# Performance work log

Hardware: AMD Instinct MI355X
Metric: run time of the kernel (lower is better)

## Reference

```python
import jax, jax.numpy as jnp
import numpy as np

EPS = 1e-5
ALPHA = 1.0

def _conv1x1(x, w, b):
    # x: [N,C,T,V], w: [O,C], b: [O] -> [N,O,T,V]
    return jnp.einsum('nctv,oc->notv', x, w) + b[None, :, None, None]

def _groupnorm1(x, gamma, beta):
    # GroupNorm(1, C): normalize over (C,T,V) per sample
    mu = jnp.mean(x, axis=(1, 2, 3), keepdims=True)
    var = jnp.var(x, axis=(1, 2, 3), keepdims=True)
    xn = (x - mu) * jax.lax.rsqrt(var + EPS)
    return xn * gamma[None, :, None, None] + beta[None, :, None, None]

def setup_inputs() -> dict:
    key = jax.random.key(0)
    ks = jax.random.split(key, 12)
    N, Cin, T, V, O, R = 128, 64, 128, 25, 64, 8
    s_in = 1.0 / np.sqrt(Cin)
    s_r = 1.0 / np.sqrt(R)
    return {
        'x':  jax.random.normal(ks[0], (N, Cin, T, V), jnp.float32),
        'A':  jax.random.normal(ks[1], (V, V), jnp.float32) * 0.1,
        'w1': jax.random.normal(ks[2], (R, Cin), jnp.float32) * s_in,
        'b1': jnp.zeros((R,), jnp.float32),
        'g1': jnp.ones((R,), jnp.float32),
        'be1': jnp.zeros((R,), jnp.float32),
        'w2': jax.random.normal(ks[3], (R, Cin), jnp.float32) * s_in,
        'b2': jnp.zeros((R,), jnp.float32),
        'g2': jnp.ones((R,), jnp.float32),
        'be2': jnp.zeros((R,), jnp.float32),
        'w3': jax.random.normal(ks[4], (O, Cin), jnp.float32) * s_in,
        'b3': jnp.zeros((O,), jnp.float32),
        'w4': jax.random.normal(ks[5], (O, R), jnp.float32) * s_r,
        'b4': jnp.zeros((O,), jnp.float32),
    }

def reference(x, A, w1, b1, g1, be1, w2, b2, g2, be2, w3, b3, w4, b4):
    # branch 1: conv1 -> GroupNorm -> temporal mean -> pairwise diff -> tanh
    x1 = _groupnorm1(_conv1x1(x, w1, b1), g1, be1).mean(axis=2)      # [N,R,V]
    y1 = jnp.tanh(x1[..., :, None] - x1[..., None, :])               # [N,R,V,V]
    # branch 2: conv2 -> GroupNorm -> temporal mean -> outer product -> tanh
    x2 = _groupnorm1(_conv1x1(x, w2, b2), g2, be2).mean(axis=2)      # [N,R,V]
    y2 = jnp.tanh(x2[..., :, None] * x2[..., None, :])               # [N,R,V,V]
    # value branch
    x3 = _conv1x1(x, w3, b3)                                          # [N,O,T,V]
    # dynamic adjacency: conv4 over rel channels
    ys = y1 + ALPHA * y2 + A[None, None]                              # [N,R,V,V]
    y_sum = jnp.einsum('nruv,or->nouv', ys, w4) + b4[None, :, None, None]
    # aggregation over vertices
    y = jnp.einsum('ncuv,nctv->nctu', y_sum, x3)                      # [N,O,T,V]
    return y
```

## Files before the change

### kernel.cpp

```cpp
#include <hip/hip_runtime.h>

#define EPSV 1e-5f
constexpr int NN = 128, CIN = 64, TT = 128, VV = 25, OO = 64, RR = 8;
constexpr int TVQ   = TT * VV;
constexpr int XSAMP = CIN * TVQ;
constexpr int YSAMP = OO * TT * VV;
constexpr int RTV   = RR * TT * VV;
constexpr int S12N  = 2 * RR * VV;
constexpr int YST_SAMP = VV * VV * OO;
constexpr int X3_SAMP  = TVQ * OO;

__global__ __launch_bounds__(256) void kZero(float* __restrict__ p, int n)
{
    int i = blockIdx.x * 256 + threadIdx.x;
    if (i < n) p[i] = 0.f;
}

__global__ __launch_bounds__(256) void kA(const float* __restrict__ x,
    const float* __restrict__ w1, const float* __restrict__ b1,
    const float* __restrict__ w2, const float* __restrict__ b2,
    float* __restrict__ s12g, float* __restrict__ ssqg)
{
    __shared__ float wt1[CIN * RR], wt2[CIN * RR];
    __shared__ float s1l[RR * VV], s2l[RR * VV];
    __shared__ float redA[4], redB[4];
    const int tid = threadIdx.x;
    const int tc  = blockIdx.x;
    const int n   = blockIdx.y;

    for (int e = tid; e < CIN * RR; e += 256) {
        int r = e >> 6, c = e & 63;
        wt1[c * RR + r] = w1[e];
        wt2[c * RR + r] = w2[e];
    }
    for (int e = tid; e < 2 * RR * VV; e += 256) {
        if (e < RR * VV) s1l[e] = 0.f; else s2l[e - RR * VV] = 0.f;
    }
    __syncthreads();

    float acc1[4][RR], acc2[4][RR];
    #pragma unroll
    for (int j = 0; j < 4; ++j)
        #pragma unroll
        for (int r = 0; r < RR; ++r) { acc1[j][r] = 0.f; acc2[j][r] = 0.f; }

    const bool active = (tid < 200);
    const int p0 = tid * 4;
    const float* xb = x + (size_t)n * XSAMP + tc * 800 + p0;
    if (active) {
        #pragma unroll 4
        for (int c = 0; c < CIN; ++c) {
            float4 xv  = *(const float4*)(xb + c * TVQ);
            float4 wa1 = *(const float4*)(&wt1[c * RR]);
            float4 wb1 = *(const float4*)(&wt1[c * RR + 4]);
            float4 wa2 = *(const float4*)(&wt2[c * RR]);
            float4 wb2 = *(const float4*)(&wt2[c * RR + 4]);
            float xj[4]  = {xv.x, xv.y, xv.z, xv.w};
            float w1v[8] = {wa1.x, wa1.y, wa1.z, wa1.w, wb1.x, wb1.y, wb1.z, wb1.w};
            float w2v[8] = {wa2.x, wa2.y, wa2.z, wa2.w, wb2.x, wb2.y, wb2.z, wb2.w};
            #pragma unroll
            for (int j = 0; j < 4; ++j)
                #pragma unroll
                for (int r = 0; r < RR; ++r) {
                    acc1[j][r] += w1v[r] * xj[j];
                    acc2[j][r] += w2v[r] * xj[j];
                }
        }
    }

    float b1r[RR], b2r[RR];
    #pragma unroll
    for (int r = 0; r < RR; ++r) { b1r[r] = b1[r]; b2r[r] = b2[r]; }

    float ssq1 = 0.f, ssq2 = 0.f;
    if (active) {
        #pragma unroll
        for (int j = 0; j < 4; ++j) {
            int v = (p0 + j) % VV;
            #pragma unroll
            for (int r = 0; r < RR; ++r) {
                float c1 = acc1[j][r] + b1r[r]; ssq1 += c1 * c1;
                float c2 = acc2[j][r] + b2r[r]; ssq2 += c2 * c2;
                atomicAdd(&s1l[r * VV + v], acc1[j][r]);
                atomicAdd(&s2l[r * VV + v], acc2[j][r]);
            }
        }
    }
    #pragma unroll
    for (int off = 32; off > 0; off >>= 1) {
        ssq1 += __shfl_down(ssq1, off);
        ssq2 += __shfl_down(ssq2, off);
    }
    if ((tid & 63) == 0) { redA[tid >> 6] = ssq1; redB[tid >> 6] = ssq2; }
    __syncthreads();
    for (int e = tid; e < S12N; e += 256) {
        float pv = (e < RR * VV) ? s1l[e] : s2l[e - RR * VV];
        atomicAdd(&s12g[n * S12N + e], pv);
    }
    if (tid == 0) {
        atomicAdd(&ssqg[n * 2 + 0], redA[0] + redA[1] + redA[2] + redA[3]);
        atomicAdd(&ssqg[n * 2 + 1], redB[0] + redB[1] + redB[2] + redB[3]);
    }
}

__device__ __forceinline__ float tanh_fast(float v)
{
    float e = __expf(2.f * v);
    return 1.f - 2.f / (e + 1.f);
}

__global__ __launch_bounds__(512) void kB(
    const float* __restrict__ s12g, const float* __restrict__ ssqg,
    const float* __restrict__ b1, const float* __restrict__ g1, const float* __restrict__ be1,
    const float* __restrict__ b2, const float* __restrict__ g2, const float* __restrict__ be2,
    const float* __restrict__ Amat, const float* __restrict__ w4, const float* __restrict__ b4,
    float* __restrict__ ysumT)
{
    __shared__ float x1g[RR * VV], x2g[RR * VV];
    __shared__ float w4l[OO * RR];
    __shared__ float b4l[OO];
    __shared__ float stats[2];
    __shared__ float mss[4];
    const int tid = threadIdx.x;
    const int bx  = blockIdx.x;
    const int n   = blockIdx.y;

    if (tid < 2) stats[tid] = 0.f;
    if (tid < OO * RR) w4l[tid] = w4[tid];
    if (tid < OO) b4l[tid] = b4[tid];
    __syncthreads();

    float sv = 0.f;
    if (tid < S12N) {
        sv = s12g[n * S12N + tid];
        atomicAdd(&stats[tid / (RR * VV)], sv);
    }
    __syncthreads();
    if (tid == 0) {
        float sb1 = 0.f, sb2 = 0.f;
        for (int r = 0; r < RR; ++r) { sb1 += b1[r]; sb2 += b2[r]; }
        float mu1 = (stats[0] + (float)(TT * VV) * sb1) / (float)RTV;
        float mu2 = (stats[1] + (float)(TT * VV) * sb2) / (float)RTV;
        float var1 = ssqg[n * 2 + 0] / (float)RTV - mu1 * mu1;
        float var2 = ssqg[n * 2 + 1] / (float)RTV - mu2 * mu2;
        mss[0] = mu1; mss[1] = rsqrtf(var1 + EPSV);
        mss[2] = mu2; mss[3] = rsqrtf(var2 + EPSV);
    }
    __syncthreads();
    if (tid < S12N) {
        int br = tid / (RR * VV);
        int i  = tid % (RR * VV);
        int r  = i / VV;
        float mu = mss[br * 2], rs = mss[br * 2 + 1];
        float mean_t = sv / (float)TT + (br ? b2[r] : b1[r]);
        float g  = br ? g2[r]  : g1[r];
        float be = br ? be2[r] : be1[r];
        float val = g * (mean_t - mu) * rs + be;
        if (br == 0) x1g[i] = val; else x2g[i] = val;
    }
    __syncthreads();

    float* yn = ysumT + (size_t)n * YST_SAMP;
    const int pend = (bx + 1) * 125;
    for (int p = bx * 125 + tid; p < pend; p += 512) {
        int u = p / VV, v = p % VV;
        float Av = Amat[p];
        float ys[RR];
        #pragma unroll
        for (int r = 0; r < RR; ++r) {
            float d = x1g[r * VV + u] - x1g[r * VV + v];
            float m = x2g[r * VV + u] * x2g[r * VV + v];
            ys[r] = tanh_fast(d) + tanh_fast(m) + Av;
        }
        float* dst = yn + (size_t)p * OO;
        for (int o = 0; o < OO; ++o) {
            float a = b4l[o];
            #pragma unroll
            for (int r = 0; r < RR; ++r) a += w4l[o * RR + r] * ys[r];
            dst[o] = a;
        }
    }
}

__global__ __launch_bounds__(256) void kC1(const float* __restrict__ x,
    const float* __restrict__ w3, const float* __restrict__ b3,
    float* __restrict__ x3T)
{
    __shared__ float wt[CIN * 68];
    const int tid = threadIdx.x;
    const int n   = blockIdx.y;
    const int oq  = tid & 7;
    const int pg  = tid >> 3;
    const int p0  = blockIdx.x * 256 + pg * 8;

    for (int e = tid; e < CIN * OO; e += 256) {
        int o = e >> 6, c = e & 63;
        wt[c * 68 + o] = w3[e];
    }
    __syncthreads();

    float acc[8][8];
    #pragma unroll
    for (int i = 0; i < 8; ++i)
        #pragma unroll
        for (int j = 0; j < 8; ++j) acc[i][j] = 0.f;

    const bool act = (p0 < TVQ);
    const float* xp = x + (size_t)n * XSAMP + p0;
    if (act) {
        #pragma unroll 4
        for (int c = 0; c < CIN; ++c) {
            const float* xc = xp + c * TVQ;
            float4 xa = *(const float4*)(xc);
            float4 xb = *(const float4*)(xc + 4);
            const float* wr = &wt[c * 68 + oq * 8];
            float4 wa = *(const float4*)(wr);
            float4 wb = *(const float4*)(wr + 4);
            float xv[8] = {xa.x, xa.y, xa.z, xa.w, xb.x, xb.y, xb.z, xb.w};
            float wv[8] = {wa.x, wa.y, wa.z, wa.w, wb.x, wb.y, wb.z, wb.w};
            #pragma unroll
            for (int i = 0; i < 8; ++i)
                #pragma unroll
                for (int j = 0; j < 8; ++j)
                    acc[i][j] += wv[i] * xv[j];
        }
    }

    float bo[8];
    #pragma unroll
    for (int i = 0; i < 8; ++i) bo[i] = b3[oq * 8 + i];
    if (act) {
        float* dst = x3T + (size_t)n * X3_SAMP + (size_t)p0 * OO + oq * 8;
        #pragma unroll
        for (int j = 0; j < 8; ++j) {
            float4 s0, s1;
            s0.x = acc[0][j] + bo[0]; s0.y = acc[1][j] + bo[1];
            s0.z = acc[2][j] + bo[2]; s0.w = acc[3][j] + bo[3];
            s1.x = acc[4][j] + bo[4]; s1.y = acc[5][j] + bo[5];
            s1.z = acc[6][j] + bo[6]; s1.w = acc[7][j] + bo[7];
            *(float4*)(dst + j * OO)     = s0;
            *(float4*)(dst + j * OO + 4) = s1;
        }
    }
}

__global__ __launch_bounds__(256) void kC2(const float* __restrict__ x3T,
    const float* __restrict__ ysumT, float* __restrict__ y)
{
    __shared__ float lds[OO * 101];
    const int tid = threadIdx.x;
    const int tc  = blockIdx.x;
    const int n   = blockIdx.y;
    const int t0  = tc * 8;
    const int o2  = tid & 63;
    const int th2 = tid >> 6;

    const float* xb = x3T + (size_t)n * X3_SAMP;
    float acc2[2][VV];
    #pragma unroll
    for (int row = 0; row < 2; ++row) {
        const int t = t0 + 2 * th2 + row;
        #pragma unroll
        for (int v = 0; v < VV; ++v)
            acc2[row][v] = xb[(size_t)(t * VV + v) * OO + o2];
    }

    const float* yT = ysumT + (size_t)n * YST_SAMP + o2;
    float res[2][VV];
    #pragma unroll
    for (int u = 0; u < VV; ++u) {
        float r0 = 0.f, r1 = 0.f;
        #pragma unroll
        for (int v = 0; v < VV; ++v) {
            float yv = yT[(u * VV + v) * OO];
            r0 += yv * acc2[0][v];
            r1 += yv * acc2[1][v];
        }
        res[0][u] = r0;
        res[1][u] = r1;
    }

    float* yb = y + (size_t)n * YSAMP + t0 * VV;
    #pragma unroll 1
    for (int half = 0; half < 2; ++half) {
        __syncthreads();
        if ((th2 >> 1) == half) {
            #pragma unroll
            for (int row = 0; row < 2; ++row) {
                const int tl = (2 * th2 + row) & 3;
                #pragma unroll
                for (int u = 0; u < VV; ++u)
                    lds[o2 * 101 + tl * VV + u] = res[row][u];
            }
        }
        __syncthreads();
        for (int e = tid; e < 6400; e += 256) {
            int o = e / 100, m = e % 100;
            yb[o * TVQ + half * 100 + m] = lds[o * 101 + m];
        }
    }
}

__global__ __launch_bounds__(256) void kC(
    const float* __restrict__ x, const float* __restrict__ w3,
    const float* __restrict__ b3, const float* __restrict__ ysumT,
    float* __restrict__ y)
{
    __shared__ float lds[7168];
    const int tid = threadIdx.x;
    const int tc  = blockIdx.x;
    const int n   = blockIdx.y;
    const int t0  = tc * 8;

    const int og = tid >> 3;
    const int th = tid & 7;
    const int o0 = og * 2;

    float acc[2][VV];
    #pragma unroll
    for (int j = 0; j < 2; ++j)
        #pragma unroll
        for (int v = 0; v < VV; ++v) acc[j][v] = 0.f;

    const float* xn = x + (size_t)n * XSAMP + t0 * VV;
    #pragma unroll 1
    for (int cpass = 0; cpass < 2; ++cpass) {
        __syncthreads();
        for (int e4 = tid; e4 < 32 * 50; e4 += 256) {
            int cl = e4 / 50, r4 = (e4 % 50) * 4;
            float4 tv = *(const float4*)(xn + (cpass * 32 + cl) * TVQ + r4);
            float a[4] = {tv.x, tv.y, tv.z, tv.w};
            #pragma unroll
            for (int j = 0; j < 4; ++j) {
                int rem = r4 + j;
                lds[cl * 224 + (rem / VV) * 28 + (rem % VV)] = a[j];
            }
        }
        __syncthreads();
        #pragma unroll 1
        for (int q = 0; q < 2; ++q) {
            float w3q[2][16];
            #pragma unroll
            for (int j = 0; j < 2; ++j)
                #pragma unroll
                for (int k4 = 0; k4 < 4; ++k4) {
                    float4 wv = *(const float4*)(w3 + (o0 + j) * CIN
                                                 + cpass * 32 + q * 16 + k4 * 4);
                    w3q[j][k4*4+0] = wv.x; w3q[j][k4*4+1] = wv.y;
                    w3q[j][k4*4+2] = wv.z; w3q[j][k4*4+3] = wv.w;
                }
            #pragma unroll
            for (int ci = 0; ci < 16; ++ci) {
                const float* p = &lds[(q * 16 + ci) * 224 + th * 28];
                float4 a0 = *(const float4*)(p + 0);
                float4 a1 = *(const float4*)(p + 4);
                float4 a2 = *(const float4*)(p + 8);
                float4 a3 = *(const float4*)(p + 12);
                float4 a4 = *(const float4*)(p + 16);
                float4 a5 = *(const float4*)(p + 20);
                float  a6 = p[24];
                #pragma unroll
                for (int j = 0; j < 2; ++j) {
                    const float w = w3q[j][ci];
                    float* a = acc[j];
                    a[0]  += w*a0.x; a[1]  += w*a0.y; a[2]  += w*a0.z; a[3]  += w*a0.w;
                    a[4]  += w*a1.x; a[5]  += w*a1.y; a[6]  += w*a1.z; a[7]  += w*a1.w;
                    a[8]  += w*a2.x; a[9]  += w*a2.y; a[10] += w*a2.z; a[11] += w*a2.w;
                    a[12] += w*a3.x; a[13] += w*a3.y; a[14] += w*a3.z; a[15] += w*a3.w;
                    a[16] += w*a4.x; a[17] += w*a4.y; a[18] += w*a4.z; a[19] += w*a4.w;
                    a[20] += w*a5.x; a[21] += w*a5.y; a[22] += w*a5.z; a[23] += w*a5.w;
                    a[24] += w*a6;
                }
            }
        }
    }

    const int o2  = tid & 63;
    const int th2 = tid >> 6;
    const float bias = b3[o2];
    float acc2[2][VV];

    #pragma unroll 1
    for (int half = 0; half < 2; ++half) {
        __syncthreads();
        if ((th >> 2) == half) {
            const int tl = th & 3;
            #pragma unroll
            for (int j = 0; j < 2; ++j)
                #pragma unroll
                for (int v = 0; v < VV; ++v)
                    lds[tl * 1601 + (o0 + j) * VV + v] = acc[j][v];
        }
        __syncthreads();
        if ((th2 >> 1) == half) {
            #pragma unroll
            for (int row = 0; row < 2; ++row) {
                const int tl = (2 * th2 + row) & 3;
                #pragma unroll
                for (int v = 0; v < VV; ++v)
                    acc2[row][v] = lds[tl * 1601 + o2 * VV + v];
            }
        }
    }
    #pragma unroll
    for (int row = 0; row < 2; ++row)
        #pragma unroll
        for (int v = 0; v < VV; ++v) acc2[row][v] += bias;

    const float* yT = ysumT + (size_t)n * YST_SAMP + o2;
    float res[2][VV];
    #pragma unroll
    for (int u = 0; u < VV; ++u) {
        float r0 = 0.f, r1 = 0.f;
        #pragma unroll
        for (int v = 0; v < VV; ++v) {
            float yv = yT[(u * VV + v) * OO];
            r0 += yv * acc2[0][v];
            r1 += yv * acc2[1][v];
        }
        res[0][u] = r0;
        res[1][u] = r1;
    }

    float* yb = y + (size_t)n * YSAMP + t0 * VV;
    #pragma unroll 1
    for (int half = 0; half < 2; ++half) {
        __syncthreads();
        if ((th2 >> 1) == half) {
            #pragma unroll
            for (int row = 0; row < 2; ++row) {
                const int tl = (2 * th2 + row) & 3;
                #pragma unroll
                for (int u = 0; u < VV; ++u)
                    lds[o2 * 101 + tl * VV + u] = res[row][u];
            }
        }
        __syncthreads();
        for (int e = tid; e < 6400; e += 256) {
            int o = e / 100, m = e % 100;
            yb[o * TVQ + half * 100 + m] = lds[o * 101 + m];
        }
    }
}

extern "C" void kernel_launch(void* const* d_in, const int* in_sizes, int n_in,
                              void* d_out, int out_size, void* d_ws, size_t ws_size,
                              hipStream_t stream)
{
    const float* x   = (const float*)d_in[0];
    const float* Am  = (const float*)d_in[1];
    const float* w1  = (const float*)d_in[2];
    const float* b1  = (const float*)d_in[3];
    const float* g1  = (const float*)d_in[4];
    const float* be1 = (const float*)d_in[5];
    const float* w2  = (const float*)d_in[6];
    const float* b2  = (const float*)d_in[7];
    const float* g2  = (const float*)d_in[8];
    const float* be2 = (const float*)d_in[9];
    const float* w3  = (const float*)d_in[10];
    const float* b3  = (const float*)d_in[11];
    const float* w4  = (const float*)d_in[12];
    const float* b4  = (const float*)d_in[13];
    float* y  = (float*)d_out;
    float* ws = (float*)d_ws;
    float* s12g  = ws;
    float* ssqg  = ws + NN * S12N;
    float* ysumT = ssqg + NN * 2;
    float* x3T   = ysumT + (size_t)NN * YST_SAMP;

    const int nz = NN * S12N + NN * 2;
    hipLaunchKernelGGL(kZero, dim3((nz + 255) / 256), dim3(256), 0, stream, ws, nz);
    hipLaunchKernelGGL(kA, dim3(4, NN), dim3(256), 0, stream,
                       x, w1, b1, w2, b2, s12g, ssqg);
    hipLaunchKernelGGL(kB, dim3(5, NN), dim3(512), 0, stream,
                       s12g, ssqg, b1, g1, be1, b2, g2, be2, Am, w4, b4, ysumT);

    const size_t baseF = (size_t)NN * S12N + NN * 2 + (size_t)NN * YST_SAMP;
    const size_t wsF   = ws_size / sizeof(float);
    long availF = (long)wsF - (long)baseF;
    int chunk = 0;
    if (availF >= (long)X3_SAMP) {
        long c = availF / (long)X3_SAMP;
        chunk = (c > NN) ? NN : (int)c;
    }
    if (chunk >= 1) {
        for (int n0 = 0; n0 < NN; n0 += chunk) {
            int nc = (NN - n0 < chunk) ? (NN - n0) : chunk;
            hipLaunchKernelGGL(kC1, dim3(13, nc), dim3(256), 0, stream,
                               x + (size_t)n0 * XSAMP, w3, b3, x3T);
            hipLaunchKernelGGL(kC2, dim3(16, nc), dim3(256), 0, stream,
                               x3T, ysumT + (size_t)n0 * YST_SAMP,
                               y + (size_t)n0 * YSAMP);
        }
    } else {
        hipLaunchKernelGGL(kC, dim3(16, NN), dim3(256), 0, stream,
                           x, w3, b3, ysumT, y);
    }
}
```

Before: 478.3 us.

## Compute GroupNorm stats via per-sample Gram matrix and pad ysum layout for vector loads

Replaces the conv1/conv2 statistics kernel with one that accumulates the 64x64 channel Gram matrix and per-vertex channel sums of x. GroupNorm mean and variance and the temporal means are then derived algebraically in kB from the weights. Separately, the ysum buffer is re-laid out as [u][o][28], zero-padded, so kC2 can read it with float4 loads. The Gram kernel does far more FLOPs and uses heavy LDS atomics, with only 2 blocks per sample, which may cost more than it saves.

```diff
diff --git a/kernel.cpp b/kernel.cpp
--- a/kernel.cpp
+++ b/kernel.cpp
@@ -5,9 +5,7 @@
 constexpr int TVQ   = TT * VV;
 constexpr int XSAMP = CIN * TVQ;
 constexpr int YSAMP = OO * TT * VV;
-constexpr int RTV   = RR * TT * VV;
-constexpr int S12N  = 2 * RR * VV;
-constexpr int YST_SAMP = VV * VV * OO;
+constexpr int YS2_SAMP = VV * OO * 28;
 constexpr int X3_SAMP  = TVQ * OO;
 
 __global__ __launch_bounds__(256) void kZero(float* __restrict__ p, int n)
@@ -16,90 +14,105 @@
     if (i < n) p[i] = 0.f;
 }
 
-__global__ __launch_bounds__(256) void kA(const float* __restrict__ x,
-    const float* __restrict__ w1, const float* __restrict__ b1,
-    const float* __restrict__ w2, const float* __restrict__ b2,
-    float* __restrict__ s12g, float* __restrict__ ssqg)
-{
-    __shared__ float wt1[CIN * RR], wt2[CIN * RR];
-    __shared__ float s1l[RR * VV], s2l[RR * VV];
-    __shared__ float redA[4], redB[4];
-    const int tid = threadIdx.x;
-    const int tc  = blockIdx.x;
-    const int n   = blockIdx.y;
-
-    for (int e = tid; e < CIN * RR; e += 256) {
-        int r = e >> 6, c = e & 63;
-        wt1[c * RR + r] = w1[e];
-        wt2[c * RR + r] = w2[e];
-    }
-    for (int e = tid; e < 2 * RR * VV; e += 256) {
-        if (e < RR * VV) s1l[e] = 0.f; else s2l[e - RR * VV] = 0.f;
-    }
-    __syncthreads();
-
-    float acc1[4][RR], acc2[4][RR];
-    #pragma unroll
-    for (int j = 0; j < 4; ++j)
-        #pragma unroll
-        for (int r = 0; r < RR; ++r) { acc1[j][r] = 0.f; acc2[j][r] = 0.f; }
-
-    const bool active = (tid < 200);
-    const int p0 = tid * 4;
-    const float* xb = x + (size_t)n * XSAMP + tc * 800 + p0;
-    if (active) {
-        #pragma unroll 4
-        for (int c = 0; c < CIN; ++c) {
-            float4 xv  = *(const float4*)(xb + c * TVQ);
-            float4 wa1 = *(const float4*)(&wt1[c * RR]);
-            float4 wb1 = *(const float4*)(&wt1[c * RR + 4]);
-            float4 wa2 = *(const float4*)(&wt2[c * RR]);
-            float4 wb2 = *(const float4*)(&wt2[c * RR + 4]);
-            float xj[4]  = {xv.x, xv.y, xv.z, xv.w};
-            float w1v[8] = {wa1.x, wa1.y, wa1.z, wa1.w, wb1.x, wb1.y, wb1.z, wb1.w};
-            float w2v[8] = {wa2.x, wa2.y, wa2.z, wa2.w, wb2.x, wb2.y, wb2.z, wb2.w};
-            #pragma unroll
-            for (int j = 0; j < 4; ++j)
-                #pragma unroll
-                for (int r = 0; r < RR; ++r) {
-                    acc1[j][r] += w1v[r] * xj[j];
-                    acc2[j][r] += w2v[r] * xj[j];
-                }
-        }
-    }
-
-    float b1r[RR], b2r[RR];
-    #pragma unroll
-    for (int r = 0; r < RR; ++r) { b1r[r] = b1[r]; b2r[r] = b2[r]; }
-
-    float ssq1 = 0.f, ssq2 = 0.f;
-    if (active) {
-        #pragma unroll
-        for (int j = 0; j < 4; ++j) {
-            int v = (p0 + j) % VV;
-            #pragma unroll
-            for (int r = 0; r < RR; ++r) {
-                float c1 = acc1[j][r] + b1r[r]; ssq1 += c1 * c1;
-                float c2 = acc2[j][r] + b2r[r]; ssq2 += c2 * c2;
-                atomicAdd(&s1l[r * VV + v], acc1[j][r]);
-                atomicAdd(&s2l[r * VV + v], acc2[j][r]);
+__global__ __launch_bounds__(256) void kG(const float* __restrict__ x,
+    float* __restrict__ Gg, float* __restrict__ xbarg)
+{
+    __shared__ float xt[4608];
+    __shared__ float bufB[64 * 68];
+    __shared__ float xbs[64 * 26];
+    const int tid  = threadIdx.x;
+    const int half = blockIdx.x;
+    const int n    = blockIdx.y;
+    const int g  = tid >> 6;
+    const int t6 = tid & 63;
+    const int ti = t6 >> 3, tj = t6 & 7;
+
+    for (int e = tid; e < 64 * 26; e += 256) xbs[e] = 0.f;
+
+    float acc[8][8];
+    #pragma unroll
+    for (int a = 0; a < 8; ++a)
+        #pragma unroll
+        for (int b = 0; b < 8; ++b) acc[a][b] = 0.f;
+
+    const float* xb = x + (size_t)n * XSAMP + half * 1600;
+    const int vbase = half * 1600;
+    #pragma unroll 1
+    for (int k = 0; k < 25; ++k) {
+        __syncthreads();
+        const int pb = k * 64;
+        for (int e = tid; e < 1024; e += 256) {
+            int c = e >> 4, p4 = e & 15;
+            float4 xv = *(const float4*)(xb + c * TVQ + pb + p4 * 4);
+            float vals[4] = {xv.x, xv.y, xv.z, xv.w};
+            #pragma unroll
+            for (int j = 0; j < 4; ++j) {
+                int p   = p4 * 4 + j;
+                int rot = (p >> 3) & 7;
+                xt[p * 72 + (((c >> 3) + rot) & 7) * 8 + (c & 7)] = vals[j];
+                int vg = (vbase + pb + p) % VV;
+                atomicAdd(&xbs[c * 26 + vg], vals[j]);
             }
         }
-    }
-    #pragma unroll
-    for (int off = 32; off > 0; off >>= 1) {
-        ssq1 += __shfl_down(ssq1, off);
-        ssq2 += __shfl_down(ssq2, off);
-    }
-    if ((tid & 63) == 0) { redA[tid >> 6] = ssq1; redB[tid >> 6] = ssq2; }
-    __syncthreads();
-    for (int e = tid; e < S12N; e += 256) {
-        float pv = (e < RR * VV) ? s1l[e] : s2l[e - RR * VV];
-        atomicAdd(&s12g[n * S12N + e], pv);
-    }
-    if (tid == 0) {
-        atomicAdd(&ssqg[n * 2 + 0], redA[0] + redA[1] + redA[2] + redA[3]);
-        atomicAdd(&ssqg[n * 2 + 1], redB[0] + redB[1] + redB[2] + redB[3]);
+        __syncthreads();
+        #pragma unroll
+        for (int pp = 0; pp < 16; ++pp) {
+            const int row = g * 16 + pp;
+            const float* xr = &xt[row * 72];
+            const int rot = (row >> 3) & 7;
+            const float* pi = xr + ((ti + rot) & 7) * 8;
+            const float* pj = xr + ((tj + rot) & 7) * 8;
+            float4 xi0 = *(const float4*)(pi);
+            float4 xi1 = *(const float4*)(pi + 4);
+            float4 xj0 = *(const float4*)(pj);
+            float4 xj1 = *(const float4*)(pj + 4);
+            float xiv[8] = {xi0.x, xi0.y, xi0.z, xi0.w, xi1.x, xi1.y, xi1.z, xi1.w};
+            float xjv[8] = {xj0.x, xj0.y, xj0.z, xj0.w, xj1.x, xj1.y, xj1.z, xj1.w};
+            #pragma unroll
+            for (int a = 0; a < 8; ++a)
+                #pragma unroll
+                for (int b = 0; b < 8; ++b)
+                    acc[a][b] += xiv[a] * xjv[b];
+        }
+    }
+    __syncthreads();
+    float* buf0 = xt;
+    if (g == 0) {
+        #pragma unroll
+        for (int a = 0; a < 8; ++a)
+            #pragma unroll
+            for (int b = 0; b < 8; ++b)
+                buf0[(ti * 8 + a) * 68 + tj * 8 + b] = acc[a][b];
+    } else if (g == 1) {
+        #pragma unroll
+        for (int a = 0; a < 8; ++a)
+            #pragma unroll
+            for (int b = 0; b < 8; ++b)
+                bufB[(ti * 8 + a) * 68 + tj * 8 + b] = acc[a][b];
+    }
+    __syncthreads();
+    if (g == 2) {
+        #pragma unroll
+        for (int a = 0; a < 8; ++a)
+            #pragma unroll
+            for (int b = 0; b < 8; ++b)
+                buf0[(ti * 8 + a) * 68 + tj * 8 + b] += acc[a][b];
+    } else if (g == 3) {
+        #pragma unroll
+        for (int a = 0; a < 8; ++a)
+            #pragma unroll
+            for (int b = 0; b < 8; ++b)
+                bufB[(ti * 8 + a) * 68 + tj * 8 + b] += acc[a][b];
+    }
+    __syncthreads();
+    for (int e = tid; e < 4096; e += 256) {
+        int r = e >> 6, cl = e & 63;
+        atomicAdd(&Gg[(size_t)n * 4096 + e],
+                  buf0[r * 68 + cl] + bufB[r * 68 + cl]);
+    }
+    for (int e = tid; e < 1600; e += 256) {
+        int c = e / VV, v = e % VV;
+        atomicAdd(&xbarg[(size_t)n * 1600 + e], xbs[c * 26 + v]);
     }
 }
 
@@ -110,57 +123,90 @@
 }
 
 __global__ __launch_bounds__(512) void kB(
-    const float* __restrict__ s12g, const float* __restrict__ ssqg,
-    const float* __restrict__ b1, const float* __restrict__ g1, const float* __restrict__ be1,
-    const float* __restrict__ b2, const float* __restrict__ g2, const float* __restrict__ be2,
-    const float* __restrict__ Amat, const float* __restrict__ w4, const float* __restrict__ b4,
-    float* __restrict__ ysumT)
+    const float* __restrict__ Gg, const float* __restrict__ xbarg,
+    const float* __restrict__ w1, const float* __restrict__ b1,
+    const float* __restrict__ g1, const float* __restrict__ be1,
+    const float* __restrict__ w2, const float* __restrict__ b2,
+    const float* __restrict__ g2, const float* __restrict__ be2,
+    const float* __restrict__ Amat, const float* __restrict__ w4,
+    const float* __restrict__ b4, float* __restrict__ ys2)
 {
     __shared__ float x1g[RR * VV], x2g[RR * VV];
     __shared__ float w4l[OO * RR];
     __shared__ float b4l[OO];
-    __shared__ float stats[2];
+    __shared__ float wl1[RR * CIN], wl2[RR * CIN];
+    __shared__ float xbl[1600];
+    __shared__ float qred[16], lin[16];
+    __shared__ float sxc[CIN];
     __shared__ float mss[4];
     const int tid = threadIdx.x;
     const int bx  = blockIdx.x;
     const int n   = blockIdx.y;
 
-    if (tid < 2) stats[tid] = 0.f;
-    if (tid < OO * RR) w4l[tid] = w4[tid];
+    if (tid < 512) { w4l[tid] = w4[tid]; wl1[tid] = w1[tid]; wl2[tid] = w2[tid]; }
     if (tid < OO) b4l[tid] = b4[tid];
-    __syncthreads();
-
-    float sv = 0.f;
-    if (tid < S12N) {
-        sv = s12g[n * S12N + tid];
-        atomicAdd(&stats[tid / (RR * VV)], sv);
-    }
-    __syncthreads();
-    if (tid == 0) {
-        float sb1 = 0.f, sb2 = 0.f;
-        for (int r = 0; r < RR; ++r) { sb1 += b1[r]; sb2 += b2[r]; }
-        float mu1 = (stats[0] + (float)(TT * VV) * sb1) / (float)RTV;
-        float mu2 = (stats[1] + (float)(TT * VV) * sb2) / (float)RTV;
-        float var1 = ssqg[n * 2 + 0] / (float)RTV - mu1 * mu1;
-        float var2 = ssqg[n * 2 + 1] / (float)RTV - mu2 * mu2;
-        mss[0] = mu1; mss[1] = rsqrtf(var1 + EPSV);
-        mss[2] = mu2; mss[3] = rsqrtf(var2 + EPSV);
-    }
-    __syncthreads();
-    if (tid < S12N) {
-        int br = tid / (RR * VV);
-        int i  = tid % (RR * VV);
-        int r  = i / VV;
-        float mu = mss[br * 2], rs = mss[br * 2 + 1];
-        float mean_t = sv / (float)TT + (br ? b2[r] : b1[r]);
-        float g  = br ? g2[r]  : g1[r];
-        float be = br ? be2[r] : be1[r];
-        float val = g * (mean_t - mu) * rs + be;
+    for (int e = tid; e < 1600; e += 512) xbl[e] = xbarg[(size_t)n * 1600 + e];
+    __syncthreads();
+
+    if (tid < CIN) {
+        float s = 0.f;
+        for (int v = 0; v < VV; ++v) s += xbl[tid * VV + v];
+        sxc[tid] = s;
+    }
+    {
+        int k = tid >> 5, ci = tid & 31;
+        int br = k >> 3, r = k & 7;
+        const float* wv = br ? wl2 : wl1;
+        const float* Gn = Gg + (size_t)n * 4096;
+        float part = 0.f;
+        #pragma unroll
+        for (int h = 0; h < 2; ++h) {
+            int c = ci + 32 * h;
+            float s = 0.f;
+            for (int cj = 0; cj < 64; ++cj) s += Gn[c * 64 + cj] * wv[r * 64 + cj];
+            part += wv[r * 64 + c] * s;
+        }
+        #pragma unroll
+        for (int off = 16; off; off >>= 1) part += __shfl_down(part, off, 32);
+        if ((tid & 31) == 0) qred[k] = part;
+    }
+    __syncthreads();
+    if (tid < 16) {
+        int br = tid >> 3, r = tid & 7;
+        const float* wv = br ? wl2 : wl1;
+        float s = 0.f;
+        for (int c = 0; c < 64; ++c) s += wv[r * 64 + c] * sxc[c];
+        lin[tid] = s;
+    }
+    __syncthreads();
+    if (tid < 2) {
+        const float* bb = tid ? b2 : b1;
+        float sl = 0.f, sq = 0.f, sb = 0.f, sb2 = 0.f;
+        for (int r = 0; r < 8; ++r) {
+            float l = lin[tid * 8 + r];
+            sl += l;
+            sq += qred[tid * 8 + r] + 2.f * bb[r] * l;
+            sb += bb[r]; sb2 += bb[r] * bb[r];
+        }
+        float mu  = (sl + 3200.f * sb) / 25600.f;
+        float var = (sq + 3200.f * sb2) / 25600.f - mu * mu;
+        mss[tid * 2]     = mu;
+        mss[tid * 2 + 1] = rsqrtf(var + EPSV);
+    }
+    __syncthreads();
+    if (tid < 400) {
+        int br = tid / 200, i = tid % 200, r = i / VV, v = i % VV;
+        const float* wv = br ? wl2 : wl1;
+        float d = 0.f;
+        for (int c = 0; c < 64; ++c) d += wv[r * 64 + c] * xbl[c * VV + v];
+        float mean_t = d * (1.f / 128.f) + (br ? b2[r] : b1[r]);
+        float val = (br ? g2[r] : g1[r]) * (mean_t - mss[br * 2]) * mss[br * 2 + 1]
+                    + (br ? be2[r] : be1[r]);
         if (br == 0) x1g[i] = val; else x2g[i] = val;
     }
     __syncthreads();
 
-    float* yn = ysumT + (size_t)n * YST_SAMP;
+    float* yn = ys2 + (size_t)n * YS2_SAMP;
     const int pend = (bx + 1) * 125;
     for (int p = bx * 125 + tid; p < pend; p += 512) {
         int u = p / VV, v = p % VV;
@@ -172,12 +218,14 @@
             float m = x2g[r * VV + u] * x2g[r * VV + v];
             ys[r] = tanh_fast(d) + tanh_fast(m) + Av;
         }
-        float* dst = yn + (size_t)p * OO;
+        float* dst = yn + u * (OO * 28) + v;
+        const bool pad = (v >= 22);
         for (int o = 0; o < OO; ++o) {
             float a = b4l[o];
             #pragma unroll
             for (int r = 0; r < RR; ++r) a += w4l[o * RR + r] * ys[r];
-            dst[o] = a;
+            dst[o * 28] = a;
+            if (pad) dst[o * 28 + 3] = 0.f;
         }
     }
 }
@@ -245,7 +293,7 @@
 }
 
 __global__ __launch_bounds__(256) void kC2(const float* __restrict__ x3T,
-    const float* __restrict__ ysumT, float* __restrict__ y)
+    const float* __restrict__ ys2, float* __restrict__ y)
 {
     __shared__ float lds[OO * 101];
     const int tid = threadIdx.x;
@@ -256,25 +304,29 @@
     const int th2 = tid >> 6;
 
     const float* xb = x3T + (size_t)n * X3_SAMP;
-    float acc2[2][VV];
+    float acc2[2][28];
     #pragma unroll
     for (int row = 0; row < 2; ++row) {
         const int t = t0 + 2 * th2 + row;
         #pragma unroll
         for (int v = 0; v < VV; ++v)
             acc2[row][v] = xb[(size_t)(t * VV + v) * OO + o2];
-    }
-
-    const float* yT = ysumT + (size_t)n * YST_SAMP + o2;
+        acc2[row][25] = 0.f; acc2[row][26] = 0.f; acc2[row][27] = 0.f;
+    }
+
+    const float* yo = ys2 + (size_t)n * YS2_SAMP + o2 * 28;
     float res[2][VV];
     #pragma unroll
     for (int u = 0; u < VV; ++u) {
+        const float* yu = yo + u * (OO * 28);
         float r0 = 0.f, r1 = 0.f;
         #pragma unroll
-        for (int v = 0; v < VV; ++v) {
-            float yv = yT[(u * VV + v) * OO];
-            r0 += yv * acc2[0][v];
-            r1 += yv * acc2[1][v];
+        for (int v4 = 0; v4 < 28; v4 += 4) {
+            float4 w = *(const float4*)(yu + v4);
+            r0 += w.x * acc2[0][v4]     + w.y * acc2[0][v4 + 1]
+                + w.z * acc2[0][v4 + 2] + w.w * acc2[0][v4 + 3];
+            r1 += w.x * acc2[1][v4]     + w.y * acc2[1][v4 + 1]
+                + w.z * acc2[1][v4 + 2] + w.w * acc2[1][v4 + 3];
         }
         res[0][u] = r0;
         res[1][u] = r1;
@@ -303,7 +355,7 @@
 
 __global__ __launch_bounds__(256) void kC(
     const float* __restrict__ x, const float* __restrict__ w3,
-    const float* __restrict__ b3, const float* __restrict__ ysumT,
+    const float* __restrict__ b3, const float* __restrict__ ys2,
     float* __restrict__ y)
 {
     __shared__ float lds[7168];
@@ -407,14 +459,14 @@
         #pragma unroll
         for (int v = 0; v < VV; ++v) acc2[row][v] += bias;
 
-    const float* yT = ysumT + (size_t)n * YST_SAMP + o2;
+    const float* yT = ys2 + (size_t)n * YS2_SAMP + o2 * 28;
     float res[2][VV];
     #pragma unroll
     for (int u = 0; u < VV; ++u) {
         float r0 = 0.f, r1 = 0.f;
         #pragma unroll
         for (int v = 0; v < VV; ++v) {
-            float yv = yT[(u * VV + v) * OO];
+            float yv = yT[u * (OO * 28) + v];
             r0 += yv * acc2[0][v];
             r1 += yv * acc2[1][v];
         }
@@ -463,19 +515,19 @@
     const float* b4  = (const float*)d_in[13];
     float* y  = (float*)d_out;
     float* ws = (float*)d_ws;
-    float* s12g  = ws;
-    float* ssqg  = ws + NN * S12N;
-    float* ysumT = ssqg + NN * 2;
-    float* x3T   = ysumT + (size_t)NN * YST_SAMP;
-
-    const int nz = NN * S12N + NN * 2;
+    float* Gg    = ws;
+    float* xbarg = Gg + (size_t)NN * 4096;
+    float* ys2   = xbarg + (size_t)NN * 1600;
+    float* x3T   = ys2 + (size_t)NN * YS2_SAMP;
+
+    const int nz = NN * 4096 + NN * 1600;
     hipLaunchKernelGGL(kZero, dim3((nz + 255) / 256), dim3(256), 0, stream, ws, nz);
-    hipLaunchKernelGGL(kA, dim3(4, NN), dim3(256), 0, stream,
-                       x, w1, b1, w2, b2, s12g, ssqg);
+    hipLaunchKernelGGL(kG, dim3(2, NN), dim3(256), 0, stream, x, Gg, xbarg);
     hipLaunchKernelGGL(kB, dim3(5, NN), dim3(512), 0, stream,
-                       s12g, ssqg, b1, g1, be1, b2, g2, be2, Am, w4, b4, ysumT);
-
-    const size_t baseF = (size_t)NN * S12N + NN * 2 + (size_t)NN * YST_SAMP;
+                       Gg, xbarg, w1, b1, g1, be1, w2, b2, g2, be2, Am, w4, b4, ys2);
+
+    const size_t baseF = (size_t)NN * 4096 + (size_t)NN * 1600
+                       + (size_t)NN * YS2_SAMP;
     const size_t wsF   = ws_size / sizeof(float);
     long availF = (long)wsF - (long)baseF;
     int chunk = 0;
@@ -489,11 +541,11 @@
             hipLaunchKernelGGL(kC1, dim3(13, nc), dim3(256), 0, stream,
                                x + (size_t)n0 * XSAMP, w3, b3, x3T);
             hipLaunchKernelGGL(kC2, dim3(16, nc), dim3(256), 0, stream,
-                               x3T, ysumT + (size_t)n0 * YST_SAMP,
+                               x3T, ys2 + (size_t)n0 * YS2_SAMP,
                                y + (size_t)n0 * YSAMP);
         }
     } else {
         hipLaunchKernelGGL(kC, dim3(16, NN), dim3(256), 0, stream,
-                           x, w3, b3, ysumT, y);
-    }
-}
+                           x, w3, b3, ys2, y);
+    }
+}
```

Result: slower. 580.4 us (+21.3%).

## Re-layout dynamic adjacency as [u][o][v] padded to 28 for float4 loads

Applied to the files above, without the earlier changes.

Changes the y_sum intermediate from [u][v][o] to [u][o][v padded to 28] so kC2 reads each thread's adjacency row with contiguous float4 loads instead of 64-float strided scalar loads. kB now runs one block per sample, staging the tanh terms for all 625 (u,v) pairs in shared memory, then writing padded rows with vectorized stores. This trades more padding bytes and a larger kB shared footprint with fewer blocks for better read vectorization in the aggregation kernel.

```diff
diff --git a/kernel.cpp b/kernel.cpp
--- a/kernel.cpp
+++ b/kernel.cpp
@@ -7,7 +7,7 @@
 constexpr int YSAMP = OO * TT * VV;
 constexpr int RTV   = RR * TT * VV;
 constexpr int S12N  = 2 * RR * VV;
-constexpr int YST_SAMP = VV * VV * OO;
+constexpr int YS2_SAMP = VV * OO * 28;
 constexpr int X3_SAMP  = TVQ * OO;
 
 __global__ __launch_bounds__(256) void kZero(float* __restrict__ p, int n)
@@ -114,19 +114,22 @@
     const float* __restrict__ b1, const float* __restrict__ g1, const float* __restrict__ be1,
     const float* __restrict__ b2, const float* __restrict__ g2, const float* __restrict__ be2,
     const float* __restrict__ Amat, const float* __restrict__ w4, const float* __restrict__ b4,
-    float* __restrict__ ysumT)
+    float* __restrict__ ys2)
 {
     __shared__ float x1g[RR * VV], x2g[RR * VV];
-    __shared__ float w4l[OO * RR];
+    __shared__ float w4t[RR * OO];
     __shared__ float b4l[OO];
+    __shared__ float ysl[625 * 9];
     __shared__ float stats[2];
     __shared__ float mss[4];
     const int tid = threadIdx.x;
-    const int bx  = blockIdx.x;
-    const int n   = blockIdx.y;
+    const int n   = blockIdx.x;
 
     if (tid < 2) stats[tid] = 0.f;
-    if (tid < OO * RR) w4l[tid] = w4[tid];
+    if (tid < OO * RR) {
+        int o = tid >> 3, r = tid & 7;
+        w4t[r * OO + o] = w4[tid];
+    }
     if (tid < OO) b4l[tid] = b4[tid];
     __syncthreads();
 
@@ -160,25 +163,43 @@
     }
     __syncthreads();
 
-    float* yn = ysumT + (size_t)n * YST_SAMP;
-    const int pend = (bx + 1) * 125;
-    for (int p = bx * 125 + tid; p < pend; p += 512) {
+    for (int p = tid; p < 625; p += 512) {
         int u = p / VV, v = p % VV;
         float Av = Amat[p];
-        float ys[RR];
         #pragma unroll
         for (int r = 0; r < RR; ++r) {
             float d = x1g[r * VV + u] - x1g[r * VV + v];
             float m = x2g[r * VV + u] * x2g[r * VV + v];
-            ys[r] = tanh_fast(d) + tanh_fast(m) + Av;
-        }
-        float* dst = yn + (size_t)p * OO;
-        for (int o = 0; o < OO; ++o) {
-            float a = b4l[o];
-            #pragma unroll
-            for (int r = 0; r < RR; ++r) a += w4l[o * RR + r] * ys[r];
-            dst[o] = a;
-        }
+            ysl[p * 9 + r] = tanh_fast(d) + tanh_fast(m) + Av;
+        }
+    }
+    __syncthreads();
+
+    float* yn = ys2 + (size_t)n * YS2_SAMP;
+    for (int e4 = tid; e4 < 11200; e4 += 512) {
+        int u   = e4 / 448;
+        int rem = e4 - u * 448;
+        int o   = rem / 7;
+        int v4  = (rem - o * 7) * 4;
+        float w[RR];
+        #pragma unroll
+        for (int r = 0; r < RR; ++r) w[r] = w4t[r * OO + o];
+        const float bb = b4l[o];
+        float4 out;
+        float* op = &out.x;
+        #pragma unroll
+        for (int j = 0; j < 4; ++j) {
+            int v = v4 + j;
+            float a = 0.f;
+            if (v < VV) {
+                a = bb;
+                const float* yr = &ysl[(u * VV + v) * 9];
+                #pragma unroll
+                for (int r = 0; r < RR; ++r) a += w[r] * yr[r];
+            }
+            op[j] = a;
+        }
+        *(float4*)(yn + u * (OO * 28) + o * 28 + v4) = out;
     }
 }
 
@@ -245,7 +266,7 @@
 }
 
 __global__ __launch_bounds__(256) void kC2(const float* __restrict__ x3T,
-    const float* __restrict__ ysumT, float* __restrict__ y)
+    const float* __restrict__ ys2, float* __restrict__ y)
 {
     __shared__ float lds[OO * 101];
     const int tid = threadIdx.x;
@@ -256,25 +277,29 @@
     const int th2 = tid >> 6;
 
     const float* xb = x3T + (size_t)n * X3_SAMP;
-    float acc2[2][VV];
+    float acc2[2][28];
     #pragma unroll
     for (int row = 0; row < 2; ++row) {
         const int t = t0 + 2 * th2 + row;
         #pragma unroll
         for (int v = 0; v < VV; ++v)
             acc2[row][v] = xb[(size_t)(t * VV + v) * OO + o2];
-    }
-
-    const float* yT = ysumT + (size_t)n * YST_SAMP + o2;
+        acc2[row][25] = 0.f; acc2[row][26] = 0.f; acc2[row][27] = 0.f;
+    }
+
+    const float* yo = ys2 + (size_t)n * YS2_SAMP + o2 * 28;
     float res[2][VV];
     #pragma unroll
     for (int u = 0; u < VV; ++u) {
+        const float* yu = yo + u * (OO * 28);
         float r0 = 0.f, r1 = 0.f;
         #pragma unroll
-        for (int v = 0; v < VV; ++v) {
-            float yv = yT[(u * VV + v) * OO];
-            r0 += yv * acc2[0][v];
-            r1 += yv * acc2[1][v];
+        for (int v4 = 0; v4 < 28; v4 += 4) {
+            float4 w = *(const float4*)(yu + v4);
+            r0 += w.x * acc2[0][v4]     + w.y * acc2[0][v4 + 1]
+                + w.z * acc2[0][v4 + 2] + w.w * acc2[0][v4 + 3];
+            r1 += w.x * acc2[1][v4]     + w.y * acc2[1][v4 + 1]
+                + w.z * acc2[1][v4 + 2] + w.w * acc2[1][v4 + 3];
         }
         res[0][u] = r0;
         res[1][u] = r1;
@@ -303,7 +328,7 @@
 
 __global__ __launch_bounds__(256) void kC(
     const float* __restrict__ x, const float* __restrict__ w3,
-    const float* __restrict__ b3, const float* __restrict__ ysumT,
+    const float* __restrict__ b3, const float* __restrict__ ys2,
     float* __restrict__ y)
 {
     __shared__ float lds[7168];
@@ -407,14 +432,14 @@
         #pragma unroll
         for (int v = 0; v < VV; ++v) acc2[row][v] += bias;
 
-    const float* yT = ysumT + (size_t)n * YST_SAMP + o2;
+    const float* yT = ys2 + (size_t)n * YS2_SAMP + o2 * 28;
     float res[2][VV];
     #pragma unroll
     for (int u = 0; u < VV; ++u) {
         float r0 = 0.f, r1 = 0.f;
         #pragma unroll
         for (int v = 0; v < VV; ++v) {
-            float yv = yT[(u * VV + v) * OO];
+            float yv = yT[u * (OO * 28) + v];
             r0 += yv * acc2[0][v];
             r1 += yv * acc2[1][v];
         }
@@ -463,19 +488,19 @@
     const float* b4  = (const float*)d_in[13];
     float* y  = (float*)d_out;
     float* ws = (float*)d_ws;
-    float* s12g  = ws;
-    float* ssqg  = ws + NN * S12N;
-    float* ysumT = ssqg + NN * 2;
-    float* x3T   = ysumT + (size_t)NN * YST_SAMP;
+    float* s12g = ws;
+    float* ssqg = s12g + (size_t)NN * S12N;
+    float* ys2  = ssqg + (size_t)NN * 2;
+    float* x3T  = ys2 + (size_t)NN * YS2_SAMP;
 
     const int nz = NN * S12N + NN * 2;
     hipLaunchKernelGGL(kZero, dim3((nz + 255) / 256), dim3(256), 0, stream, ws, nz);
     hipLaunchKernelGGL(kA, dim3(4, NN), dim3(256), 0, stream,
                        x, w1, b1, w2, b2, s12g, ssqg);
-    hipLaunchKernelGGL(kB, dim3(5, NN), dim3(512), 0, stream,
-                       s12g, ssqg, b1, g1, be1, b2, g2, be2, Am, w4, b4, ysumT);
-
-    const size_t baseF = (size_t)NN * S12N + NN * 2 + (size_t)NN * YST_SAMP;
+    hipLaunchKernelGGL(kB, dim3(NN), dim3(512), 0, stream,
+                       s12g, ssqg, b1, g1, be1, b2, g2, be2, Am, w4, b4, ys2);
+
+    const size_t baseF = (size_t)NN * S12N + NN * 2 + (size_t)NN * YS2_SAMP;
     const size_t wsF   = ws_size / sizeof(float);
     long availF = (long)wsF - (long)baseF;
     int chunk = 0;
@@ -489,11 +514,11 @@
             hipLaunchKernelGGL(kC1, dim3(13, nc), dim3(256), 0, stream,
                                x + (size_t)n0 * XSAMP, w3, b3, x3T);
             hipLaunchKernelGGL(kC2, dim3(16, nc), dim3(256), 0, stream,
-                               x3T, ysumT + (size_t)n0 * YST_SAMP,
+                               x3T, ys2 + (size_t)n0 * YS2_SAMP,
                                y + (size_t)n0 * YSAMP);
         }
     } else {
         hipLaunchKernelGGL(kC, dim3(16, NN), dim3(256), 0, stream,
-                           x, w3, b3, ysumT, y);
-    }
-}
+                           x, w3, b3, ys2, y);
+    }
+}
```

Measured after the change: 453.9 us. 5.1% less time.
